# Kernel optimization log

Hardware: AMD Instinct MI355X
Metric: run time of the kernel (lower is better)

The kernel has to match this reference:

```python
import jax, jax.numpy as jnp
import numpy as np

N_NODES, N_EDGES, D_FEAT, HIDDEN, N_CLASSES = 100000, 3200000, 128, 16, 40


def setup_inputs() -> dict:
    key = jax.random.key(0)
    ks = jax.random.split(key, 6)
    x = jax.random.normal(ks[0], (N_NODES, D_FEAT), dtype=jnp.float32)
    edge_index = jax.random.randint(ks[1], (2, N_EDGES), 0, N_NODES, dtype=jnp.int32)
    # SAGEConv params: lin_l (aggregated neighbors, with bias), lin_r (root, no bias)
    W_l = jax.random.normal(ks[2], (D_FEAT, HIDDEN), dtype=jnp.float32) / np.sqrt(D_FEAT)
    b_l = jnp.zeros((HIDDEN,), jnp.float32)
    W_r = jax.random.normal(ks[3], (D_FEAT, HIDDEN), dtype=jnp.float32) / np.sqrt(D_FEAT)
    # final Linear(hidden, num_classes)
    W3 = jax.random.normal(ks[4], (HIDDEN, N_CLASSES), dtype=jnp.float32) / np.sqrt(HIDDEN)
    b3 = jnp.zeros((N_CLASSES,), jnp.float32)
    return {"x": x, "edge_index": edge_index, "W_l": W_l, "b_l": b_l,
            "W_r": W_r, "W3": W3, "b3": b3}


def reference(x, edge_index, W_l, b_l, W_r, W3, b3):
    N = x.shape[0]
    src, dst = edge_index[0], edge_index[1]
    # mean aggregation of source features onto target nodes (PyG source_to_target)
    agg = jax.ops.segment_sum(x[src], dst, num_segments=N)            # [N, F]
    deg = jax.ops.segment_sum(jnp.ones_like(dst, dtype=x.dtype), dst, num_segments=N)
    mean = agg / jnp.maximum(deg, 1.0)[:, None]                        # zero-in-degree -> 0
    # SAGEConv: lin_l(mean) + lin_r(x)
    h = mean @ W_l + b_l + x @ W_r                                     # [N, 16]
    h = jax.nn.relu(h)
    logits = h @ W3 + b3                                               # [N, C]
    return jax.nn.log_softmax(logits, axis=1)
```

## Files before the change

### kernel.cpp

```cpp
#include <hip/hip_runtime.h>
#include <hip/hip_bf16.h>

#define D_FEAT 128
#define HIDDEN 16
#define NCLS 40
#define EPB 4096
#define QSCALE 32.0f
#define QBIAS  8.0f

typedef unsigned int uint;

__device__ __forceinline__ void fma4(float4& a, float s, const float4 w) {
  a.x += s * w.x; a.y += s * w.y; a.z += s * w.z; a.w += s * w.w;
}

__global__ __launch_bounds__(256) void p1lin_kernel(
    const int* __restrict__ src, const int* __restrict__ dst,
    int* __restrict__ gcur1, int* __restrict__ buf1,
    int E, int C, int R1, int nb1,
    const float* __restrict__ x,
    const float* __restrict__ Wl, const float* __restrict__ Wr,
    uint* __restrict__ ylb, float* __restrict__ yr, int N) {
  __shared__ __align__(16) char smem[20880];
  int tid = threadIdx.x;

  if ((int)blockIdx.x < nb1) {
    int* lbuf  = (int*)smem;
    unsigned char* skey = (unsigned char*)(smem + 16384);
    int* lh    = (int*)(smem + 20480);
    int* loff  = lh + 32;
    int* gbase = loff + 33;
    if (tid < 32) lh[tid] = 0;
    __syncthreads();

    int base = blockIdx.x * EPB;
    int key[16], rnk[16], rec[16];
#pragma unroll
    for (int j = 0; j < 16; ++j) {
      int e = base + j * 256 + tid;
      bool ok = e < E;
      int d = ok ? dst[e] : 0;
      int s = ok ? src[e] : 0;
      key[j] = ok ? (d >> 12) : -1;
      rec[j] = s | ((d & 4095) << 17);
      if (ok) rnk[j] = atomicAdd(&lh[key[j]], 1);
    }
    __syncthreads();

    if (tid < 64) {
      int v = (tid < 32) ? lh[tid] : 0;
      int inc = v;
#pragma unroll
      for (int dd = 1; dd < 32; dd <<= 1) {
        int t = __shfl_up(inc, dd);
        if ((int)tid >= dd) inc += t;
      }
      if (tid < 32) {
        loff[tid] = inc - v;
        gbase[tid] = (v && tid < C) ? atomicAdd(&gcur1[tid], v) : 0;
      }
    }
    __syncthreads();

#pragma unroll
    for (int j = 0; j < 16; ++j) {
      if (key[j] >= 0) {
        int p = loff[key[j]] + rnk[j];
        lbuf[p] = rec[j];
        skey[p] = (unsigned char)key[j];
      }
    }
    __syncthreads();

    int tot = min(EPB, E - base);
    for (int i = tid; i < tot; i += 256) {
      int r = lbuf[i];
      int k = skey[i];
      int gp = gbase[k] + (i - loff[k]);
      if (gp < R1) buf1[(size_t)k * R1 + gp] = r;
    }
  } else {
    float* sW = (float*)smem;
    const float4* sWf4 = (const float4*)smem;

    for (int i = tid; i < 4096; i += 256) {
      int k = i >> 5, c = i & 31;
      sW[i] = (c < 16) ? Wl[k * 16 + c] : Wr[k * 16 + (c - 16)];
    }
    __syncthreads();

    int row0 = ((int)blockIdx.x - nb1) * 128;
    int quad = tid & 7, rg = tid >> 3;
    int r0 = row0 + rg * 4;
    int rr0 = min(r0 + 0, N - 1), rr1 = min(r0 + 1, N - 1);
    int rr2 = min(r0 + 2, N - 1), rr3 = min(r0 + 3, N - 1);
    const float* xp0 = x + (size_t)rr0 * D_FEAT;
    const float* xp1 = x + (size_t)rr1 * D_FEAT;
    const float* xp2 = x + (size_t)rr2 * D_FEAT;
    const float* xp3 = x + (size_t)rr3 * D_FEAT;

    float4 acc0 = {0,0,0,0}, acc1 = {0,0,0,0}, acc2 = {0,0,0,0}, acc3 = {0,0,0,0};
#pragma unroll 4
    for (int k4 = 0; k4 < 32; ++k4) {
      float4 x0 = *(const float4*)(xp0 + k4 * 4);
      float4 x1 = *(const float4*)(xp1 + k4 * 4);
      float4 x2 = *(const float4*)(xp2 + k4 * 4);
      float4 x3 = *(const float4*)(xp3 + k4 * 4);
      float4 w0 = sWf4[(k4 * 4 + 0) * 8 + quad];
      fma4(acc0, x0.x, w0); fma4(acc1, x1.x, w0);
      fma4(acc2, x2.x, w0); fma4(acc3, x3.x, w0);
      float4 w1 = sWf4[(k4 * 4 + 1) * 8 + quad];
      fma4(acc0, x0.y, w1); fma4(acc1, x1.y, w1);
      fma4(acc2, x2.y, w1); fma4(acc3, x3.y, w1);
      float4 w2 = sWf4[(k4 * 4 + 2) * 8 + quad];
      fma4(acc0, x0.z, w2); fma4(acc1, x1.z, w2);
      fma4(acc2, x2.z, w2); fma4(acc3, x3.z, w2);
      float4 w3 = sWf4[(k4 * 4 + 3) * 8 + quad];
      fma4(acc0, x0.w, w3); fma4(acc1, x1.w, w3);
      fma4(acc2, x2.w, w3); fma4(acc3, x3.w, w3);
    }

    float4 accs[4] = {acc0, acc1, acc2, acc3};
    if (quad < 4) {
#pragma unroll
      for (int r = 0; r < 4; ++r) {
        if (r0 + r < N) {
          float4 a = accs[r];
          int q0 = __float2int_rn((fminf(fmaxf(a.x, -7.9f), 7.9f) + QBIAS) * QSCALE);
          int q1 = __float2int_rn((fminf(fmaxf(a.y, -7.9f), 7.9f) + QBIAS) * QSCALE);
          int q2 = __float2int_rn((fminf(fmaxf(a.z, -7.9f), 7.9f) + QBIAS) * QSCALE);
          int q3 = __float2int_rn((fminf(fmaxf(a.w, -7.9f), 7.9f) + QBIAS) * QSCALE);
          uint2 pk;
          pk.x = (uint)q0 | ((uint)q1 << 16);
          pk.y = (uint)q2 | ((uint)q3 << 16);
          *(uint2*)(ylb + (size_t)(r0 + r) * 8 + quad * 2) = pk;
        }
      }
    } else {
#pragma unroll
      for (int r = 0; r < 4; ++r) {
        if (r0 + r < N)
          *(float4*)(yr + (size_t)(r0 + r) * 16 + (quad - 4) * 4) = accs[r];
      }
    }
  }
}

__global__ __launch_bounds__(256) void pass2_kernel(
    const int* __restrict__ buf1, const int* __restrict__ gcur1,
    int* __restrict__ gcur, int* __restrict__ packed,
    int C, int R1, int RF, int chunks) {
  __shared__ int lbuf[EPB];
  __shared__ int lh[32], loff[32], gbase[32];

  int c = blockIdx.x / chunks;
  int chunk = blockIdx.x - c * chunks;
  int cnt1 = min(gcur1[c], R1);
  int base = chunk * EPB;
  int tot = cnt1 - base;
  if (tot <= 0) return;
  tot = min(tot, EPB);

  int tid = threadIdx.x;
  if (tid < 32) lh[tid] = 0;
  __syncthreads();

  const int* in = buf1 + (size_t)c * R1 + base;
  int key[16], rnk[16], rec[16];
#pragma unroll
  for (int j = 0; j < 16; ++j) {
    int i = j * 256 + tid;
    bool ok = i < tot;
    int r = ok ? in[i] : 0;
    key[j] = ok ? ((r >> 24) & 31) : -1;
    rec[j] = r;
    if (ok) rnk[j] = atomicAdd(&lh[key[j]], 1);
  }
  __syncthreads();

  if (tid < 64) {
    int v = (tid < 32) ? lh[tid] : 0;
    int inc = v;
#pragma unroll
    for (int dd = 1; dd < 32; dd <<= 1) {
      int t = __shfl_up(inc, dd);
      if ((int)tid >= dd) inc += t;
    }
    if (tid < 32) {
      loff[tid] = inc - v;
      gbase[tid] = v ? atomicAdd(&gcur[c * 32 + tid], v) : 0;
    }
  }
  __syncthreads();

#pragma unroll
  for (int j = 0; j < 16; ++j)
    if (key[j] >= 0) lbuf[loff[key[j]] + rnk[j]] = rec[j];
  __syncthreads();

  for (int i = tid; i < tot; i += 256) {
    int r = lbuf[i];
    int k = (r >> 24) & 31;
    int gp = gbase[k] + (i - loff[k]);
    if (gp < RF) {
      int d12 = (r >> 17) & 4095;
      packed[(size_t)(c * 32 + k) * RF + gp] =
          (r & 0x1FFFF) | ((d12 & 127) << 20);
    }
  }
}

__global__ __launch_bounds__(1024) void baggrf_kernel(
    const uint* __restrict__ ylb, const int* __restrict__ packed,
    const int* __restrict__ gcur, const float* __restrict__ yr,
    const float* __restrict__ bl, const float* __restrict__ W3,
    const float* __restrict__ b3, float* __restrict__ out,
    int N, int RF) {
  __shared__ uint sagg[128 * 9];
  __shared__ int sdeg[128];
  __shared__ float syr[128 * 16];
  __shared__ float sW3[16 * NCLS];
  __shared__ float sb3[NCLS];
  __shared__ float sbl[16];
  int tid = threadIdx.x;
  int b = blockIdx.x;
  int node0 = b * 128;

  for (int i = tid; i < 128 * 9; i += 1024) sagg[i] = 0u;
  if (tid < 128) sdeg[tid] = 0;
  if (tid >= 384 && tid < 1024) sW3[tid - 384] = W3[tid - 384];
  if (tid < NCLS) sb3[tid] = b3[tid];
  if (tid >= 64 && tid < 80) sbl[tid - 64] = bl[tid - 64];
  __syncthreads();

  int cnt = min(gcur[b], RF);
  int lo = b * RF, hi = lo + cnt;
  for (int e0 = lo + tid; e0 < hi; e0 += 4096) {
    int e1 = e0 + 1024, e2 = e0 + 2048, e3 = e0 + 3072;
    bool h1 = e1 < hi, h2 = e2 < hi, h3 = e3 < hi;
    int p0 = packed[e0];
    int p1 = packed[h1 ? e1 : e0];
    int p2 = packed[h2 ? e2 : e0];
    int p3 = packed[h3 ? e3 : e0];
    int s0 = p0 & 0xFFFFF, d0 = (p0 >> 20) & 127;
    int s1 = p1 & 0xFFFFF, d1 = (p1 >> 20) & 127;
    int s2 = p2 & 0xFFFFF, d2 = (p2 >> 20) & 127;
    int s3 = p3 & 0xFFFFF, d3 = (p3 >> 20) & 127;
    const uint4* q0 = (const uint4*)(ylb + (size_t)s0 * 8);
    const uint4* q1 = (const uint4*)(ylb + (size_t)s1 * 8);
    const uint4* q2 = (const uint4*)(ylb + (size_t)s2 * 8);
    const uint4* q3 = (const uint4*)(ylb + (size_t)s3 * 8);
    uint4 a0 = q0[0], a1 = q0[1];
    uint4 b0 = q1[0], b1 = q1[1];
    uint4 c0 = q2[0], c1 = q2[1];
    uint4 e4 = q3[0], e5 = q3[1];

    uint* ip0 = &sagg[d0 * 9];
    atomicAdd(ip0 + 0, a0.x); atomicAdd(ip0 + 1, a0.y);
    atomicAdd(ip0 + 2, a0.z); atomicAdd(ip0 + 3, a0.w);
    atomicAdd(ip0 + 4, a1.x); atomicAdd(ip0 + 5, a1.y);
    atomicAdd(ip0 + 6, a1.z); atomicAdd(ip0 + 7, a1.w);
    atomicAdd(&sdeg[d0], 1);
    if (h1) {
      uint* ip = &sagg[d1 * 9];
      atomicAdd(ip + 0, b0.x); atomicAdd(ip + 1, b0.y);
      atomicAdd(ip + 2, b0.z); atomicAdd(ip + 3, b0.w);
      atomicAdd(ip + 4, b1.x); atomicAdd(ip + 5, b1.y);
      atomicAdd(ip + 6, b1.z); atomicAdd(ip + 7, b1.w);
      atomicAdd(&sdeg[d1], 1);
    }
    if (h2) {
      uint* ip = &sagg[d2 * 9];
      atomicAdd(ip + 0, c0.x); atomicAdd(ip + 1, c0.y);
      atomicAdd(ip + 2, c0.z); atomicAdd(ip + 3, c0.w);
      atomicAdd(ip + 4, c1.x); atomicAdd(ip + 5, c1.y);
      atomicAdd(ip + 6, c1.z); atomicAdd(ip + 7, c1.w);
      atomicAdd(&sdeg[d2], 1);
    }
    if (h3) {
      uint* ip = &sagg[d3 * 9];
      atomicAdd(ip + 0, e4.x); atomicAdd(ip + 1, e4.y);
      atomicAdd(ip + 2, e4.z); atomicAdd(ip + 3, e4.w);
      atomicAdd(ip + 4, e5.x); atomicAdd(ip + 5, e5.y);
      atomicAdd(ip + 6, e5.z); atomicAdd(ip + 7, e5.w);
      atomicAdd(&sdeg[d3], 1);
    }
  }

  int nvalid = min(128, N - node0);
  if (nvalid > 0) {
    int tot16 = nvalid * 16;
    for (int i = tid; i < tot16; i += 1024)
      syr[i] = yr[(size_t)node0 * 16 + i];
  }
  __syncthreads();

  int node = tid >> 3, q = tid & 7;
  int n = node0 + node;
  if (n < N) {
    int dg = sdeg[node];
    float bsub = (QBIAS * QSCALE) * (float)dg;
    float inv = 1.0f / (QSCALE * fmaxf((float)dg, 1.0f));
    float h[16];
#pragma unroll
    for (int j = 0; j < 8; ++j) {
      uint s = sagg[node * 9 + j];
      float v0 = ((float)(s & 0xFFFFu) - bsub) * inv;
      float v1 = ((float)(s >> 16) - bsub) * inv;
      h[2 * j]     = fmaxf(v0 + sbl[2 * j]     + syr[node * 16 + 2 * j], 0.f);
      h[2 * j + 1] = fmaxf(v1 + sbl[2 * j + 1] + syr[node * 16 + 2 * j + 1], 0.f);
    }
    float lg[5];
#pragma unroll
    for (int j = 0; j < 5; ++j) lg[j] = sb3[q * 5 + j];
#pragma unroll
    for (int k = 0; k < 16; ++k) {
      float hv = h[k];
#pragma unroll
      for (int j = 0; j < 5; ++j) lg[j] += hv * sW3[k * NCLS + q * 5 + j];
    }
    float m = lg[0];
#pragma unroll
    for (int j = 1; j < 5; ++j) m = fmaxf(m, lg[j]);
#pragma unroll
    for (int dd = 1; dd < 8; dd <<= 1) m = fmaxf(m, __shfl_xor(m, dd));
    float s = 0.f;
#pragma unroll
    for (int j = 0; j < 5; ++j) s += __expf(lg[j] - m);
#pragma unroll
    for (int dd = 1; dd < 8; dd <<= 1) s += __shfl_xor(s, dd);
    float lse = m + __logf(s);
    float* op = out + (size_t)n * NCLS + q * 5;
#pragma unroll
    for (int j = 0; j < 5; ++j) op[j] = lg[j] - lse;
  }
}

extern "C" void kernel_launch(void* const* d_in, const int* in_sizes, int n_in,
                              void* d_out, int out_size, void* d_ws, size_t ws_size,
                              hipStream_t stream) {
  const float* x   = (const float*)d_in[0];
  const int* eidx  = (const int*)d_in[1];
  const float* Wl  = (const float*)d_in[2];
  const float* bl  = (const float*)d_in[3];
  const float* Wr  = (const float*)d_in[4];
  const float* W3  = (const float*)d_in[5];
  const float* b3  = (const float*)d_in[6];
  float* out = (float*)d_out;

  int N = in_sizes[0] / D_FEAT;
  int E = in_sizes[1] / 2;
  const int* src = eidx;
  const int* dst = eidx + E;

  int C = (N + 4095) >> 12;
  int chunks = (E / C) / EPB + 2;
  int R1 = chunks * EPB;
  int Bf = C * 32;
  int B = (N + 127) >> 7;
  long long m = (long long)E * 128 / N;
  int RF = (int)((m + m / 8 + 511) / 512 * 512);

  size_t n16 = (size_t)N * 16;
  uint* ylb   = (uint*)d_ws;
  float* yr   = (float*)(ylb + (size_t)N * 8);
  int* gcur   = (int*)(yr + n16);
  int* gcur1  = gcur + Bf;
  int* buf1   = gcur1 + C;
  int* packed = buf1 + (size_t)C * R1;

  hipMemsetAsync(gcur, 0, (size_t)(Bf + C) * sizeof(int), stream);

  int nb1 = (E + EPB - 1) / EPB;
  int nblin = (N + 127) / 128;
  p1lin_kernel<<<nb1 + nblin, 256, 0, stream>>>(src, dst, gcur1, buf1,
                                                E, C, R1, nb1,
                                                x, Wl, Wr, ylb, yr, N);

  pass2_kernel<<<C * chunks, 256, 0, stream>>>(buf1, gcur1, gcur, packed,
                                               C, R1, RF, chunks);

  baggrf_kernel<<<B, 1024, 0, stream>>>(ylb, packed, gcur, yr, bl, W3, b3,
                                        out, N, RF);
}
```

Measured before the change: 98.86 us.

## Split fused partition/linear kernel into separate pass1 and lin kernels

Undoes the fusion of the edge-partition pass and the dense linear projection, launching them as two separate kernels. The partition kernel now precomputes each edge's global destination index in shared memory instead of storing a byte key and recomputing offsets in the scatter loop. The lin kernel gets a launch-bounds occupancy hint. Separate launches drop the shared-memory union and let each kernel use its own resources, at the cost of losing concurrency between the two phases and adding one launch.

```diff
diff --git a/kernel.cpp b/kernel.cpp
--- a/kernel.cpp
+++ b/kernel.cpp
@@ -14,134 +14,130 @@
   a.x += s * w.x; a.y += s * w.y; a.z += s * w.z; a.w += s * w.w;
 }
 
-__global__ __launch_bounds__(256) void p1lin_kernel(
+__global__ __launch_bounds__(256) void pass1_kernel(
     const int* __restrict__ src, const int* __restrict__ dst,
     int* __restrict__ gcur1, int* __restrict__ buf1,
-    int E, int C, int R1, int nb1,
+    int E, int C, int R1) {
+  __shared__ int lh[32], loff[32], gbase[32];
+  __shared__ int lbuf[EPB];
+  __shared__ int ldst[EPB];
+  int tid = threadIdx.x;
+  if (tid < 32) lh[tid] = 0;
+  __syncthreads();
+
+  int base = blockIdx.x * EPB;
+  int key[16], rnk[16], rec[16];
+#pragma unroll
+  for (int j = 0; j < 16; ++j) {
+    int e = base + j * 256 + tid;
+    bool ok = e < E;
+    int d = ok ? dst[e] : 0;
+    int s = ok ? src[e] : 0;
+    key[j] = ok ? (d >> 12) : -1;
+    rec[j] = s | ((d & 4095) << 17);
+    if (ok) rnk[j] = atomicAdd(&lh[key[j]], 1);
+  }
+  __syncthreads();
+
+  if (tid < 64) {
+    int v = (tid < 32) ? lh[tid] : 0;
+    int inc = v;
+#pragma unroll
+    for (int dd = 1; dd < 32; dd <<= 1) {
+      int t = __shfl_up(inc, dd);
+      if ((int)tid >= dd) inc += t;
+    }
+    if (tid < 32) {
+      loff[tid] = inc - v;
+      gbase[tid] = (v && tid < C) ? atomicAdd(&gcur1[tid], v) : 0;
+    }
+  }
+  __syncthreads();
+
+#pragma unroll
+  for (int j = 0; j < 16; ++j) {
+    if (key[j] >= 0) {
+      int p = loff[key[j]] + rnk[j];
+      lbuf[p] = rec[j];
+      int gp = gbase[key[j]] + rnk[j];
+      ldst[p] = (gp < R1) ? key[j] * R1 + gp : -1;
+    }
+  }
+  __syncthreads();
+
+  int tot = min(EPB, E - base);
+  for (int i = tid; i < tot; i += 256) {
+    int di = ldst[i];
+    if (di >= 0) buf1[di] = lbuf[i];
+  }
+}
+
+__global__ __launch_bounds__(256, 6) void lin_kernel(
     const float* __restrict__ x,
     const float* __restrict__ Wl, const float* __restrict__ Wr,
     uint* __restrict__ ylb, float* __restrict__ yr, int N) {
-  __shared__ __align__(16) char smem[20880];
+  __shared__ float sW[4096];
+  const float4* sWf4 = (const float4*)sW;
   int tid = threadIdx.x;
 
-  if ((int)blockIdx.x < nb1) {
-    int* lbuf  = (int*)smem;
-    unsigned char* skey = (unsigned char*)(smem + 16384);
-    int* lh    = (int*)(smem + 20480);
-    int* loff  = lh + 32;
-    int* gbase = loff + 33;
-    if (tid < 32) lh[tid] = 0;
-    __syncthreads();
-
-    int base = blockIdx.x * EPB;
-    int key[16], rnk[16], rec[16];
-#pragma unroll
-    for (int j = 0; j < 16; ++j) {
-      int e = base + j * 256 + tid;
-      bool ok = e < E;
-      int d = ok ? dst[e] : 0;
-      int s = ok ? src[e] : 0;
-      key[j] = ok ? (d >> 12) : -1;
-      rec[j] = s | ((d & 4095) << 17);
-      if (ok) rnk[j] = atomicAdd(&lh[key[j]], 1);
-    }
-    __syncthreads();
-
-    if (tid < 64) {
-      int v = (tid < 32) ? lh[tid] : 0;
-      int inc = v;
-#pragma unroll
-      for (int dd = 1; dd < 32; dd <<= 1) {
-        int t = __shfl_up(inc, dd);
-        if ((int)tid >= dd) inc += t;
+  for (int i = tid; i < 4096; i += 256) {
+    int k = i >> 5, c = i & 31;
+    sW[i] = (c < 16) ? Wl[k * 16 + c] : Wr[k * 16 + (c - 16)];
+  }
+  __syncthreads();
+
+  int row0 = blockIdx.x * 128;
+  int quad = tid & 7, rg = tid >> 3;
+  int r0 = row0 + rg * 4;
+  int rr0 = min(r0 + 0, N - 1), rr1 = min(r0 + 1, N - 1);
+  int rr2 = min(r0 + 2, N - 1), rr3 = min(r0 + 3, N - 1);
+  const float* xp0 = x + (size_t)rr0 * D_FEAT;
+  const float* xp1 = x + (size_t)rr1 * D_FEAT;
+  const float* xp2 = x + (size_t)rr2 * D_FEAT;
+  const float* xp3 = x + (size_t)rr3 * D_FEAT;
+
+  float4 acc0 = {0,0,0,0}, acc1 = {0,0,0,0}, acc2 = {0,0,0,0}, acc3 = {0,0,0,0};
+#pragma unroll 4
+  for (int k4 = 0; k4 < 32; ++k4) {
+    float4 x0 = *(const float4*)(xp0 + k4 * 4);
+    float4 x1 = *(const float4*)(xp1 + k4 * 4);
+    float4 x2 = *(const float4*)(xp2 + k4 * 4);
+    float4 x3 = *(const float4*)(xp3 + k4 * 4);
+    float4 w0 = sWf4[(k4 * 4 + 0) * 8 + quad];
+    fma4(acc0, x0.x, w0); fma4(acc1, x1.x, w0);
+    fma4(acc2, x2.x, w0); fma4(acc3, x3.x, w0);
+    float4 w1 = sWf4[(k4 * 4 + 1) * 8 + quad];
+    fma4(acc0, x0.y, w1); fma4(acc1, x1.y, w1);
+    fma4(acc2, x2.y, w1); fma4(acc3, x3.y, w1);
+    float4 w2 = sWf4[(k4 * 4 + 2) * 8 + quad];
+    fma4(acc0, x0.z, w2); fma4(acc1, x1.z, w2);
+    fma4(acc2, x2.z, w2); fma4(acc3, x3.z, w2);
+    float4 w3 = sWf4[(k4 * 4 + 3) * 8 + quad];
+    fma4(acc0, x0.w, w3); fma4(acc1, x1.w, w3);
+    fma4(acc2, x2.w, w3); fma4(acc3, x3.w, w3);
+  }
+
+  float4 accs[4] = {acc0, acc1, acc2, acc3};
+  if (quad < 4) {
+#pragma unroll
+    for (int r = 0; r < 4; ++r) {
+      if (r0 + r < N) {
+        float4 a = accs[r];
+        int q0 = __float2int_rn((fminf(fmaxf(a.x, -7.9f), 7.9f) + QBIAS) * QSCALE);
+        int q1 = __float2int_rn((fminf(fmaxf(a.y, -7.9f), 7.9f) + QBIAS) * QSCALE);
+        int q2 = __float2int_rn((fminf(fmaxf(a.z, -7.9f), 7.9f) + QBIAS) * QSCALE);
+        int q3 = __float2int_rn((fminf(fmaxf(a.w, -7.9f), 7.9f) + QBIAS) * QSCALE);
+        uint2 pk;
+        pk.x = (uint)q0 | ((uint)q1 << 16);
+        pk.y = (uint)q2 | ((uint)q3 << 16);
+        *(uint2*)(ylb + (size_t)(r0 + r) * 8 + quad * 2) = pk;
       }
-      if (tid < 32) {
-        loff[tid] = inc - v;
-        gbase[tid] = (v && tid < C) ? atomicAdd(&gcur1[tid], v) : 0;
-      }
-    }
-    __syncthreads();
-
-#pragma unroll
-    for (int j = 0; j < 16; ++j) {
-      if (key[j] >= 0) {
-        int p = loff[key[j]] + rnk[j];
-        lbuf[p] = rec[j];
-        skey[p] = (unsigned char)key[j];
-      }
-    }
-    __syncthreads();
-
-    int tot = min(EPB, E - base);
-    for (int i = tid; i < tot; i += 256) {
-      int r = lbuf[i];
-      int k = skey[i];
-      int gp = gbase[k] + (i - loff[k]);
-      if (gp < R1) buf1[(size_t)k * R1 + gp] = r;
     }
   } else {
-    float* sW = (float*)smem;
-    const float4* sWf4 = (const float4*)smem;
-
-    for (int i = tid; i < 4096; i += 256) {
-      int k = i >> 5, c = i & 31;
-      sW[i] = (c < 16) ? Wl[k * 16 + c] : Wr[k * 16 + (c - 16)];
-    }
-    __syncthreads();
-
-    int row0 = ((int)blockIdx.x - nb1) * 128;
-    int quad = tid & 7, rg = tid >> 3;
-    int r0 = row0 + rg * 4;
-    int rr0 = min(r0 + 0, N - 1), rr1 = min(r0 + 1, N - 1);
-    int rr2 = min(r0 + 2, N - 1), rr3 = min(r0 + 3, N - 1);
-    const float* xp0 = x + (size_t)rr0 * D_FEAT;
-    const float* xp1 = x + (size_t)rr1 * D_FEAT;
-    const float* xp2 = x + (size_t)rr2 * D_FEAT;
-    const float* xp3 = x + (size_t)rr3 * D_FEAT;
-
-    float4 acc0 = {0,0,0,0}, acc1 = {0,0,0,0}, acc2 = {0,0,0,0}, acc3 = {0,0,0,0};
-#pragma unroll 4
-    for (int k4 = 0; k4 < 32; ++k4) {
-      float4 x0 = *(const float4*)(xp0 + k4 * 4);
-      float4 x1 = *(const float4*)(xp1 + k4 * 4);
-      float4 x2 = *(const float4*)(xp2 + k4 * 4);
-      float4 x3 = *(const float4*)(xp3 + k4 * 4);
-      float4 w0 = sWf4[(k4 * 4 + 0) * 8 + quad];
-      fma4(acc0, x0.x, w0); fma4(acc1, x1.x, w0);
-      fma4(acc2, x2.x, w0); fma4(acc3, x3.x, w0);
-      float4 w1 = sWf4[(k4 * 4 + 1) * 8 + quad];
-      fma4(acc0, x0.y, w1); fma4(acc1, x1.y, w1);
-      fma4(acc2, x2.y, w1); fma4(acc3, x3.y, w1);
-      float4 w2 = sWf4[(k4 * 4 + 2) * 8 + quad];
-      fma4(acc0, x0.z, w2); fma4(acc1, x1.z, w2);
-      fma4(acc2, x2.z, w2); fma4(acc3, x3.z, w2);
-      float4 w3 = sWf4[(k4 * 4 + 3) * 8 + quad];
-      fma4(acc0, x0.w, w3); fma4(acc1, x1.w, w3);
-      fma4(acc2, x2.w, w3); fma4(acc3, x3.w, w3);
-    }
-
-    float4 accs[4] = {acc0, acc1, acc2, acc3};
-    if (quad < 4) {
-#pragma unroll
-      for (int r = 0; r < 4; ++r) {
-        if (r0 + r < N) {
-          float4 a = accs[r];
-          int q0 = __float2int_rn((fminf(fmaxf(a.x, -7.9f), 7.9f) + QBIAS) * QSCALE);
-          int q1 = __float2int_rn((fminf(fmaxf(a.y, -7.9f), 7.9f) + QBIAS) * QSCALE);
-          int q2 = __float2int_rn((fminf(fmaxf(a.z, -7.9f), 7.9f) + QBIAS) * QSCALE);
-          int q3 = __float2int_rn((fminf(fmaxf(a.w, -7.9f), 7.9f) + QBIAS) * QSCALE);
-          uint2 pk;
-          pk.x = (uint)q0 | ((uint)q1 << 16);
-          pk.y = (uint)q2 | ((uint)q3 << 16);
-          *(uint2*)(ylb + (size_t)(r0 + r) * 8 + quad * 2) = pk;
-        }
-      }
-    } else {
-#pragma unroll
-      for (int r = 0; r < 4; ++r) {
-        if (r0 + r < N)
-          *(float4*)(yr + (size_t)(r0 + r) * 16 + (quad - 4) * 4) = accs[r];
-      }
+#pragma unroll
+    for (int r = 0; r < 4; ++r) {
+      if (r0 + r < N)
+        *(float4*)(yr + (size_t)(r0 + r) * 16 + (quad - 4) * 4) = accs[r];
     }
   }
 }
@@ -372,10 +368,10 @@
   hipMemsetAsync(gcur, 0, (size_t)(Bf + C) * sizeof(int), stream);
 
   int nb1 = (E + EPB - 1) / EPB;
+  pass1_kernel<<<nb1, 256, 0, stream>>>(src, dst, gcur1, buf1, E, C, R1);
+
   int nblin = (N + 127) / 128;
-  p1lin_kernel<<<nb1 + nblin, 256, 0, stream>>>(src, dst, gcur1, buf1,
-                                                E, C, R1, nb1,
-                                                x, Wl, Wr, ylb, yr, N);
+  lin_kernel<<<nblin, 256, 0, stream>>>(x, Wl, Wr, ylb, yr, N);
 
   pass2_kernel<<<C * chunks, 256, 0, stream>>>(buf1, gcur1, gcur, packed,
                                                C, R1, RF, chunks);
```

Result: slower. 105.4 us (+6.6%).

## Fuse three-kernel pipeline into one persistent cooperative kernel with grid syncs

Applied to the files above, without the earlier changes.

Replaces the memset and the three separate launches (bucket pass 1 plus linear, pass 2, aggregate-and-finalize) with a single cooperative persistent kernel. It uses 1024-thread blocks that loop over work items and separates the stages with grid-wide syncs. Tile sizes change as well: EPB doubles and linear tiles grow to 512 rows. This removes launch gaps and the memset, but adds grid.sync overhead, caps the grid at 512 blocks, and 1024-thread blocks may reduce occupancy or load balance.

```diff
diff --git a/kernel.cpp b/kernel.cpp
--- a/kernel.cpp
+++ b/kernel.cpp
@@ -1,10 +1,12 @@
 #include <hip/hip_runtime.h>
+#include <hip/hip_cooperative_groups.h>
 #include <hip/hip_bf16.h>
 
+namespace cg = cooperative_groups;
+
 #define D_FEAT 128
-#define HIDDEN 16
 #define NCLS 40
-#define EPB 4096
+#define EPB 8192
 #define QSCALE 32.0f
 #define QBIAS  8.0f
 
@@ -14,35 +16,182 @@
   a.x += s * w.x; a.y += s * w.y; a.z += s * w.z; a.w += s * w.w;
 }
 
-__global__ __launch_bounds__(256) void p1lin_kernel(
+__global__ __launch_bounds__(1024, 8) void mega_kernel(
     const int* __restrict__ src, const int* __restrict__ dst,
-    int* __restrict__ gcur1, int* __restrict__ buf1,
-    int E, int C, int R1, int nb1,
     const float* __restrict__ x,
     const float* __restrict__ Wl, const float* __restrict__ Wr,
-    uint* __restrict__ ylb, float* __restrict__ yr, int N) {
-  __shared__ __align__(16) char smem[20880];
+    const float* __restrict__ bl, const float* __restrict__ W3,
+    const float* __restrict__ b3,
+    uint* __restrict__ ylb, float* __restrict__ yr,
+    int* __restrict__ gcur, int* __restrict__ gcur1,
+    int* __restrict__ buf1, int* __restrict__ packed,
+    float* __restrict__ out,
+    int N, int E, int C, int R1, int RF, int chunks2,
+    int nb1, int nblin, int nItem2, int nItem3) {
+  cg::grid_group grid = cg::this_grid();
+  __shared__ __align__(16) char smem[41472];
   int tid = threadIdx.x;
-
-  if ((int)blockIdx.x < nb1) {
-    int* lbuf  = (int*)smem;
-    unsigned char* skey = (unsigned char*)(smem + 16384);
-    int* lh    = (int*)(smem + 20480);
-    int* loff  = lh + 32;
-    int* gbase = loff + 33;
+  int bid = blockIdx.x;
+  int nBlk = gridDim.x;
+
+  if (bid == 0) {
+    int tot = C * 32 + C;
+    for (int i = tid; i < tot; i += 1024) gcur[i] = 0;
+  }
+  grid.sync();
+
+  int nItem1 = nb1 + nblin;
+  for (int it = bid; it < nItem1; it += nBlk) {
+    if (it < nb1) {
+      int* lbuf = (int*)smem;
+      unsigned char* skey = (unsigned char*)(smem + 32768);
+      int* lh = (int*)(smem + 40960);
+      int* loff = lh + 32;
+      int* gbase = loff + 32;
+      if (tid < 32) lh[tid] = 0;
+      __syncthreads();
+
+      int base = it * EPB;
+      int key[8], rnk[8], rec[8];
+#pragma unroll
+      for (int j = 0; j < 8; ++j) {
+        int e = base + j * 1024 + tid;
+        bool ok = e < E;
+        int d = ok ? dst[e] : 0;
+        int s = ok ? src[e] : 0;
+        key[j] = ok ? (d >> 12) : -1;
+        rec[j] = s | ((d & 4095) << 17);
+        if (ok) rnk[j] = atomicAdd(&lh[key[j]], 1);
+      }
+      __syncthreads();
+
+      if (tid < 64) {
+        int v = (tid < 32) ? lh[tid] : 0;
+        int inc = v;
+#pragma unroll
+        for (int dd = 1; dd < 32; dd <<= 1) {
+          int t = __shfl_up(inc, dd);
+          if ((int)tid >= dd) inc += t;
+        }
+        if (tid < 32) {
+          loff[tid] = inc - v;
+          gbase[tid] = (v && tid < C) ? atomicAdd(&gcur1[tid], v) : 0;
+        }
+      }
+      __syncthreads();
+
+#pragma unroll
+      for (int j = 0; j < 8; ++j) {
+        if (key[j] >= 0) {
+          int p = loff[key[j]] + rnk[j];
+          lbuf[p] = rec[j];
+          skey[p] = (unsigned char)key[j];
+        }
+      }
+      __syncthreads();
+
+      int tot = min(EPB, E - base);
+      for (int i = tid; i < tot; i += 1024) {
+        int r = lbuf[i];
+        int k = skey[i];
+        int gp = gbase[k] + (i - loff[k]);
+        if (gp < R1) buf1[(size_t)k * R1 + gp] = r;
+      }
+      __syncthreads();
+    } else {
+      float* sW = (float*)smem;
+      const float4* sWf4 = (const float4*)smem;
+      for (int i = tid; i < 4096; i += 1024) {
+        int k = i >> 5, c = i & 31;
+        sW[i] = (c < 16) ? Wl[k * 16 + c] : Wr[k * 16 + (c - 16)];
+      }
+      __syncthreads();
+
+      int row0 = (it - nb1) * 512;
+      int quad = tid & 7, rg = tid >> 3;
+      int r0 = row0 + rg * 4;
+      int rr0 = min(r0 + 0, N - 1), rr1 = min(r0 + 1, N - 1);
+      int rr2 = min(r0 + 2, N - 1), rr3 = min(r0 + 3, N - 1);
+      const float* xp0 = x + (size_t)rr0 * D_FEAT;
+      const float* xp1 = x + (size_t)rr1 * D_FEAT;
+      const float* xp2 = x + (size_t)rr2 * D_FEAT;
+      const float* xp3 = x + (size_t)rr3 * D_FEAT;
+
+      float4 acc0 = {0,0,0,0}, acc1 = {0,0,0,0};
+      float4 acc2 = {0,0,0,0}, acc3 = {0,0,0,0};
+#pragma unroll 4
+      for (int k4 = 0; k4 < 32; ++k4) {
+        float4 x0 = *(const float4*)(xp0 + k4 * 4);
+        float4 x1 = *(const float4*)(xp1 + k4 * 4);
+        float4 x2 = *(const float4*)(xp2 + k4 * 4);
+        float4 x3 = *(const float4*)(xp3 + k4 * 4);
+        float4 w0 = sWf4[(k4 * 4 + 0) * 8 + quad];
+        fma4(acc0, x0.x, w0); fma4(acc1, x1.x, w0);
+        fma4(acc2, x2.x, w0); fma4(acc3, x3.x, w0);
+        float4 w1 = sWf4[(k4 * 4 + 1) * 8 + quad];
+        fma4(acc0, x0.y, w1); fma4(acc1, x1.y, w1);
+        fma4(acc2, x2.y, w1); fma4(acc3, x3.y, w1);
+        float4 w2 = sWf4[(k4 * 4 + 2) * 8 + quad];
+        fma4(acc0, x0.z, w2); fma4(acc1, x1.z, w2);
+        fma4(acc2, x2.z, w2); fma4(acc3, x3.z, w2);
+        float4 w3 = sWf4[(k4 * 4 + 3) * 8 + quad];
+        fma4(acc0, x0.w, w3); fma4(acc1, x1.w, w3);
+        fma4(acc2, x2.w, w3); fma4(acc3, x3.w, w3);
+      }
+
+      float4 accs[4] = {acc0, acc1, acc2, acc3};
+      if (quad < 4) {
+#pragma unroll
+        for (int r = 0; r < 4; ++r) {
+          if (r0 + r < N) {
+            float4 a = accs[r];
+            int q0 = __float2int_rn((fminf(fmaxf(a.x, -7.9f), 7.9f) + QBIAS) * QSCALE);
+            int q1 = __float2int_rn((fminf(fmaxf(a.y, -7.9f), 7.9f) + QBIAS) * QSCALE);
+            int q2 = __float2int_rn((fminf(fmaxf(a.z, -7.9f), 7.9f) + QBIAS) * QSCALE);
+            int q3 = __float2int_rn((fminf(fmaxf(a.w, -7.9f), 7.9f) + QBIAS) * QSCALE);
+            uint2 pk;
+            pk.x = (uint)q0 | ((uint)q1 << 16);
+            pk.y = (uint)q2 | ((uint)q3 << 16);
+            *(uint2*)(ylb + (size_t)(r0 + r) * 8 + quad * 2) = pk;
+          }
+        }
+      } else {
+#pragma unroll
+        for (int r = 0; r < 4; ++r) {
+          if (r0 + r < N)
+            *(float4*)(yr + (size_t)(r0 + r) * 16 + (quad - 4) * 4) = accs[r];
+        }
+      }
+      __syncthreads();
+    }
+  }
+  grid.sync();
+
+  for (int it = bid; it < nItem2; it += nBlk) {
+    int c = it / chunks2;
+    int chunk = it - c * chunks2;
+    int cnt1 = min(gcur1[c], R1);
+    int base = chunk * EPB;
+    int tot = cnt1 - base;
+    if (tot <= 0) continue;
+    tot = min(tot, EPB);
+
+    int* lbuf = (int*)smem;
+    int* lh = (int*)(smem + 40960);
+    int* loff = lh + 32;
+    int* gbase = loff + 32;
     if (tid < 32) lh[tid] = 0;
     __syncthreads();
 
-    int base = blockIdx.x * EPB;
-    int key[16], rnk[16], rec[16];
-#pragma unroll
-    for (int j = 0; j < 16; ++j) {
-      int e = base + j * 256 + tid;
-      bool ok = e < E;
-      int d = ok ? dst[e] : 0;
-      int s = ok ? src[e] : 0;
-      key[j] = ok ? (d >> 12) : -1;
-      rec[j] = s | ((d & 4095) << 17);
+    const int* in = buf1 + (size_t)c * R1 + base;
+    int key[8], rnk[8], rec[8];
+#pragma unroll
+    for (int j = 0; j < 8; ++j) {
+      int i = j * 1024 + tid;
+      bool ok = i < tot;
+      int r = ok ? in[i] : 0;
+      key[j] = ok ? ((r >> 24) & 31) : -1;
+      rec[j] = r;
       if (ok) rnk[j] = atomicAdd(&lh[key[j]], 1);
     }
     __syncthreads();
@@ -57,290 +206,156 @@
       }
       if (tid < 32) {
         loff[tid] = inc - v;
-        gbase[tid] = (v && tid < C) ? atomicAdd(&gcur1[tid], v) : 0;
-      }
-    }
-    __syncthreads();
-
-#pragma unroll
-    for (int j = 0; j < 16; ++j) {
-      if (key[j] >= 0) {
-        int p = loff[key[j]] + rnk[j];
-        lbuf[p] = rec[j];
-        skey[p] = (unsigned char)key[j];
-      }
-    }
-    __syncthreads();
-
-    int tot = min(EPB, E - base);
-    for (int i = tid; i < tot; i += 256) {
+        gbase[tid] = v ? atomicAdd(&gcur[c * 32 + tid], v) : 0;
+      }
+    }
+    __syncthreads();
+
+#pragma unroll
+    for (int j = 0; j < 8; ++j)
+      if (key[j] >= 0) lbuf[loff[key[j]] + rnk[j]] = rec[j];
+    __syncthreads();
+
+    for (int i = tid; i < tot; i += 1024) {
       int r = lbuf[i];
-      int k = skey[i];
+      int k = (r >> 24) & 31;
       int gp = gbase[k] + (i - loff[k]);
-      if (gp < R1) buf1[(size_t)k * R1 + gp] = r;
-    }
-  } else {
-    float* sW = (float*)smem;
-    const float4* sWf4 = (const float4*)smem;
-
-    for (int i = tid; i < 4096; i += 256) {
-      int k = i >> 5, c = i & 31;
-      sW[i] = (c < 16) ? Wl[k * 16 + c] : Wr[k * 16 + (c - 16)];
-    }
-    __syncthreads();
-
-    int row0 = ((int)blockIdx.x - nb1) * 128;
-    int quad = tid & 7, rg = tid >> 3;
-    int r0 = row0 + rg * 4;
-    int rr0 = min(r0 + 0, N - 1), rr1 = min(r0 + 1, N - 1);
-    int rr2 = min(r0 + 2, N - 1), rr3 = min(r0 + 3, N - 1);
-    const float* xp0 = x + (size_t)rr0 * D_FEAT;
-    const float* xp1 = x + (size_t)rr1 * D_FEAT;
-    const float* xp2 = x + (size_t)rr2 * D_FEAT;
-    const float* xp3 = x + (size_t)rr3 * D_FEAT;
-
-    float4 acc0 = {0,0,0,0}, acc1 = {0,0,0,0}, acc2 = {0,0,0,0}, acc3 = {0,0,0,0};
-#pragma unroll 4
-    for (int k4 = 0; k4 < 32; ++k4) {
-      float4 x0 = *(const float4*)(xp0 + k4 * 4);
-      float4 x1 = *(const float4*)(xp1 + k4 * 4);
-      float4 x2 = *(const float4*)(xp2 + k4 * 4);
-      float4 x3 = *(const float4*)(xp3 + k4 * 4);
-      float4 w0 = sWf4[(k4 * 4 + 0) * 8 + quad];
-      fma4(acc0, x0.x, w0); fma4(acc1, x1.x, w0);
-      fma4(acc2, x2.x, w0); fma4(acc3, x3.x, w0);
-      float4 w1 = sWf4[(k4 * 4 + 1) * 8 + quad];
-      fma4(acc0, x0.y, w1); fma4(acc1, x1.y, w1);
-      fma4(acc2, x2.y, w1); fma4(acc3, x3.y, w1);
-      float4 w2 = sWf4[(k4 * 4 + 2) * 8 + quad];
-      fma4(acc0, x0.z, w2); fma4(acc1, x1.z, w2);
-      fma4(acc2, x2.z, w2); fma4(acc3, x3.z, w2);
-      float4 w3 = sWf4[(k4 * 4 + 3) * 8 + quad];
-      fma4(acc0, x0.w, w3); fma4(acc1, x1.w, w3);
-      fma4(acc2, x2.w, w3); fma4(acc3, x3.w, w3);
-    }
-
-    float4 accs[4] = {acc0, acc1, acc2, acc3};
-    if (quad < 4) {
-#pragma unroll
-      for (int r = 0; r < 4; ++r) {
-        if (r0 + r < N) {
-          float4 a = accs[r];
-          int q0 = __float2int_rn((fminf(fmaxf(a.x, -7.9f), 7.9f) + QBIAS) * QSCALE);
-          int q1 = __float2int_rn((fminf(fmaxf(a.y, -7.9f), 7.9f) + QBIAS) * QSCALE);
-          int q2 = __float2int_rn((fminf(fmaxf(a.z, -7.9f), 7.9f) + QBIAS) * QSCALE);
-          int q3 = __float2int_rn((fminf(fmaxf(a.w, -7.9f), 7.9f) + QBIAS) * QSCALE);
-          uint2 pk;
-          pk.x = (uint)q0 | ((uint)q1 << 16);
-          pk.y = (uint)q2 | ((uint)q3 << 16);
-          *(uint2*)(ylb + (size_t)(r0 + r) * 8 + quad * 2) = pk;
-        }
-      }
-    } else {
-#pragma unroll
-      for (int r = 0; r < 4; ++r) {
-        if (r0 + r < N)
-          *(float4*)(yr + (size_t)(r0 + r) * 16 + (quad - 4) * 4) = accs[r];
-      }
-    }
+      if (gp < RF) {
+        int d12 = (r >> 17) & 4095;
+        packed[(size_t)(c * 32 + k) * RF + gp] =
+            (r & 0x1FFFF) | ((d12 & 127) << 20);
+      }
+    }
+    __syncthreads();
   }
-}
-
-__global__ __launch_bounds__(256) void pass2_kernel(
-    const int* __restrict__ buf1, const int* __restrict__ gcur1,
-    int* __restrict__ gcur, int* __restrict__ packed,
-    int C, int R1, int RF, int chunks) {
-  __shared__ int lbuf[EPB];
-  __shared__ int lh[32], loff[32], gbase[32];
-
-  int c = blockIdx.x / chunks;
-  int chunk = blockIdx.x - c * chunks;
-  int cnt1 = min(gcur1[c], R1);
-  int base = chunk * EPB;
-  int tot = cnt1 - base;
-  if (tot <= 0) return;
-  tot = min(tot, EPB);
-
-  int tid = threadIdx.x;
-  if (tid < 32) lh[tid] = 0;
-  __syncthreads();
-
-  const int* in = buf1 + (size_t)c * R1 + base;
-  int key[16], rnk[16], rec[16];
-#pragma unroll
-  for (int j = 0; j < 16; ++j) {
-    int i = j * 256 + tid;
-    bool ok = i < tot;
-    int r = ok ? in[i] : 0;
-    key[j] = ok ? ((r >> 24) & 31) : -1;
-    rec[j] = r;
-    if (ok) rnk[j] = atomicAdd(&lh[key[j]], 1);
-  }
-  __syncthreads();
-
-  if (tid < 64) {
-    int v = (tid < 32) ? lh[tid] : 0;
-    int inc = v;
-#pragma unroll
-    for (int dd = 1; dd < 32; dd <<= 1) {
-      int t = __shfl_up(inc, dd);
-      if ((int)tid >= dd) inc += t;
-    }
-    if (tid < 32) {
-      loff[tid] = inc - v;
-      gbase[tid] = v ? atomicAdd(&gcur[c * 32 + tid], v) : 0;
-    }
-  }
-  __syncthreads();
-
-#pragma unroll
-  for (int j = 0; j < 16; ++j)
-    if (key[j] >= 0) lbuf[loff[key[j]] + rnk[j]] = rec[j];
-  __syncthreads();
-
-  for (int i = tid; i < tot; i += 256) {
-    int r = lbuf[i];
-    int k = (r >> 24) & 31;
-    int gp = gbase[k] + (i - loff[k]);
-    if (gp < RF) {
-      int d12 = (r >> 17) & 4095;
-      packed[(size_t)(c * 32 + k) * RF + gp] =
-          (r & 0x1FFFF) | ((d12 & 127) << 20);
-    }
-  }
-}
-
-__global__ __launch_bounds__(1024) void baggrf_kernel(
-    const uint* __restrict__ ylb, const int* __restrict__ packed,
-    const int* __restrict__ gcur, const float* __restrict__ yr,
-    const float* __restrict__ bl, const float* __restrict__ W3,
-    const float* __restrict__ b3, float* __restrict__ out,
-    int N, int RF) {
-  __shared__ uint sagg[128 * 9];
-  __shared__ int sdeg[128];
-  __shared__ float syr[128 * 16];
-  __shared__ float sW3[16 * NCLS];
-  __shared__ float sb3[NCLS];
-  __shared__ float sbl[16];
-  int tid = threadIdx.x;
-  int b = blockIdx.x;
-  int node0 = b * 128;
-
-  for (int i = tid; i < 128 * 9; i += 1024) sagg[i] = 0u;
-  if (tid < 128) sdeg[tid] = 0;
-  if (tid >= 384 && tid < 1024) sW3[tid - 384] = W3[tid - 384];
-  if (tid < NCLS) sb3[tid] = b3[tid];
-  if (tid >= 64 && tid < 80) sbl[tid - 64] = bl[tid - 64];
-  __syncthreads();
-
-  int cnt = min(gcur[b], RF);
-  int lo = b * RF, hi = lo + cnt;
-  for (int e0 = lo + tid; e0 < hi; e0 += 4096) {
-    int e1 = e0 + 1024, e2 = e0 + 2048, e3 = e0 + 3072;
-    bool h1 = e1 < hi, h2 = e2 < hi, h3 = e3 < hi;
-    int p0 = packed[e0];
-    int p1 = packed[h1 ? e1 : e0];
-    int p2 = packed[h2 ? e2 : e0];
-    int p3 = packed[h3 ? e3 : e0];
-    int s0 = p0 & 0xFFFFF, d0 = (p0 >> 20) & 127;
-    int s1 = p1 & 0xFFFFF, d1 = (p1 >> 20) & 127;
-    int s2 = p2 & 0xFFFFF, d2 = (p2 >> 20) & 127;
-    int s3 = p3 & 0xFFFFF, d3 = (p3 >> 20) & 127;
-    const uint4* q0 = (const uint4*)(ylb + (size_t)s0 * 8);
-    const uint4* q1 = (const uint4*)(ylb + (size_t)s1 * 8);
-    const uint4* q2 = (const uint4*)(ylb + (size_t)s2 * 8);
-    const uint4* q3 = (const uint4*)(ylb + (size_t)s3 * 8);
-    uint4 a0 = q0[0], a1 = q0[1];
-    uint4 b0 = q1[0], b1 = q1[1];
-    uint4 c0 = q2[0], c1 = q2[1];
-    uint4 e4 = q3[0], e5 = q3[1];
-
-    uint* ip0 = &sagg[d0 * 9];
-    atomicAdd(ip0 + 0, a0.x); atomicAdd(ip0 + 1, a0.y);
-    atomicAdd(ip0 + 2, a0.z); atomicAdd(ip0 + 3, a0.w);
-    atomicAdd(ip0 + 4, a1.x); atomicAdd(ip0 + 5, a1.y);
-    atomicAdd(ip0 + 6, a1.z); atomicAdd(ip0 + 7, a1.w);
-    atomicAdd(&sdeg[d0], 1);
-    if (h1) {
-      uint* ip = &sagg[d1 * 9];
-      atomicAdd(ip + 0, b0.x); atomicAdd(ip + 1, b0.y);
-      atomicAdd(ip + 2, b0.z); atomicAdd(ip + 3, b0.w);
-      atomicAdd(ip + 4, b1.x); atomicAdd(ip + 5, b1.y);
-      atomicAdd(ip + 6, b1.z); atomicAdd(ip + 7, b1.w);
-      atomicAdd(&sdeg[d1], 1);
-    }
-    if (h2) {
-      uint* ip = &sagg[d2 * 9];
-      atomicAdd(ip + 0, c0.x); atomicAdd(ip + 1, c0.y);
-      atomicAdd(ip + 2, c0.z); atomicAdd(ip + 3, c0.w);
-      atomicAdd(ip + 4, c1.x); atomicAdd(ip + 5, c1.y);
-      atomicAdd(ip + 6, c1.z); atomicAdd(ip + 7, c1.w);
-      atomicAdd(&sdeg[d2], 1);
-    }
-    if (h3) {
-      uint* ip = &sagg[d3 * 9];
-      atomicAdd(ip + 0, e4.x); atomicAdd(ip + 1, e4.y);
-      atomicAdd(ip + 2, e4.z); atomicAdd(ip + 3, e4.w);
-      atomicAdd(ip + 4, e5.x); atomicAdd(ip + 5, e5.y);
-      atomicAdd(ip + 6, e5.z); atomicAdd(ip + 7, e5.w);
-      atomicAdd(&sdeg[d3], 1);
-    }
-  }
-
-  int nvalid = min(128, N - node0);
-  if (nvalid > 0) {
-    int tot16 = nvalid * 16;
-    for (int i = tid; i < tot16; i += 1024)
-      syr[i] = yr[(size_t)node0 * 16 + i];
-  }
-  __syncthreads();
-
-  int node = tid >> 3, q = tid & 7;
-  int n = node0 + node;
-  if (n < N) {
-    int dg = sdeg[node];
-    float bsub = (QBIAS * QSCALE) * (float)dg;
-    float inv = 1.0f / (QSCALE * fmaxf((float)dg, 1.0f));
-    float h[16];
-#pragma unroll
-    for (int j = 0; j < 8; ++j) {
-      uint s = sagg[node * 9 + j];
-      float v0 = ((float)(s & 0xFFFFu) - bsub) * inv;
-      float v1 = ((float)(s >> 16) - bsub) * inv;
-      h[2 * j]     = fmaxf(v0 + sbl[2 * j]     + syr[node * 16 + 2 * j], 0.f);
-      h[2 * j + 1] = fmaxf(v1 + sbl[2 * j + 1] + syr[node * 16 + 2 * j + 1], 0.f);
-    }
-    float lg[5];
-#pragma unroll
-    for (int j = 0; j < 5; ++j) lg[j] = sb3[q * 5 + j];
-#pragma unroll
-    for (int k = 0; k < 16; ++k) {
-      float hv = h[k];
-#pragma unroll
-      for (int j = 0; j < 5; ++j) lg[j] += hv * sW3[k * NCLS + q * 5 + j];
-    }
-    float m = lg[0];
-#pragma unroll
-    for (int j = 1; j < 5; ++j) m = fmaxf(m, lg[j]);
-#pragma unroll
-    for (int dd = 1; dd < 8; dd <<= 1) m = fmaxf(m, __shfl_xor(m, dd));
-    float s = 0.f;
-#pragma unroll
-    for (int j = 0; j < 5; ++j) s += __expf(lg[j] - m);
-#pragma unroll
-    for (int dd = 1; dd < 8; dd <<= 1) s += __shfl_xor(s, dd);
-    float lse = m + __logf(s);
-    float* op = out + (size_t)n * NCLS + q * 5;
-#pragma unroll
-    for (int j = 0; j < 5; ++j) op[j] = lg[j] - lse;
+  grid.sync();
+
+  for (int it = bid; it < nItem3; it += nBlk) {
+    uint* sagg = (uint*)smem;
+    int* sdeg = (int*)(smem + 4608);
+    float* syr = (float*)(smem + 5120);
+    float* sW3 = (float*)(smem + 13312);
+    float* sb3 = (float*)(smem + 15872);
+    float* sbl = (float*)(smem + 16032);
+    int node0 = it * 128;
+
+    for (int i = tid; i < 128 * 9; i += 1024) sagg[i] = 0u;
+    if (tid < 128) sdeg[tid] = 0;
+    if (tid >= 384 && tid < 1024) sW3[tid - 384] = W3[tid - 384];
+    if (tid < NCLS) sb3[tid] = b3[tid];
+    if (tid >= 64 && tid < 80) sbl[tid - 64] = bl[tid - 64];
+    __syncthreads();
+
+    int cnt = min(gcur[it], RF);
+    int lo = it * RF, hi = lo + cnt;
+    for (int e0 = lo + tid; e0 < hi; e0 += 4096) {
+      int e1 = e0 + 1024, e2 = e0 + 2048, e3 = e0 + 3072;
+      bool h1 = e1 < hi, h2 = e2 < hi, h3 = e3 < hi;
+      int p0 = packed[e0];
+      int p1 = packed[h1 ? e1 : e0];
+      int p2 = packed[h2 ? e2 : e0];
+      int p3 = packed[h3 ? e3 : e0];
+      int s0 = p0 & 0xFFFFF, d0 = (p0 >> 20) & 127;
+      int s1 = p1 & 0xFFFFF, d1 = (p1 >> 20) & 127;
+      int s2 = p2 & 0xFFFFF, d2 = (p2 >> 20) & 127;
+      int s3 = p3 & 0xFFFFF, d3 = (p3 >> 20) & 127;
+      const uint4* q0 = (const uint4*)(ylb + (size_t)s0 * 8);
+      const uint4* q1 = (const uint4*)(ylb + (size_t)s1 * 8);
+      const uint4* q2 = (const uint4*)(ylb + (size_t)s2 * 8);
+      const uint4* q3 = (const uint4*)(ylb + (size_t)s3 * 8);
+      uint4 a0 = q0[0], a1 = q0[1];
+      uint4 b0 = q1[0], b1 = q1[1];
+      uint4 c0 = q2[0], c1 = q2[1];
+      uint4 e4 = q3[0], e5 = q3[1];
+
+      uint* ip0 = &sagg[d0 * 9];
+      atomicAdd(ip0 + 0, a0.x); atomicAdd(ip0 + 1, a0.y);
+      atomicAdd(ip0 + 2, a0.z); atomicAdd(ip0 + 3, a0.w);
+      atomicAdd(ip0 + 4, a1.x); atomicAdd(ip0 + 5, a1.y);
+      atomicAdd(ip0 + 6, a1.z); atomicAdd(ip0 + 7, a1.w);
+      atomicAdd(&sdeg[d0], 1);
+      if (h1) {
+        uint* ip = &sagg[d1 * 9];
+        atomicAdd(ip + 0, b0.x); atomicAdd(ip + 1, b0.y);
+        atomicAdd(ip + 2, b0.z); atomicAdd(ip + 3, b0.w);
+        atomicAdd(ip + 4, b1.x); atomicAdd(ip + 5, b1.y);
+        atomicAdd(ip + 6, b1.z); atomicAdd(ip + 7, b1.w);
+        atomicAdd(&sdeg[d1], 1);
+      }
+      if (h2) {
+        uint* ip = &sagg[d2 * 9];
+        atomicAdd(ip + 0, c0.x); atomicAdd(ip + 1, c0.y);
+        atomicAdd(ip + 2, c0.z); atomicAdd(ip + 3, c0.w);
+        atomicAdd(ip + 4, c1.x); atomicAdd(ip + 5, c1.y);
+        atomicAdd(ip + 6, c1.z); atomicAdd(ip + 7, c1.w);
+        atomicAdd(&sdeg[d2], 1);
+      }
+      if (h3) {
+        uint* ip = &sagg[d3 * 9];
+        atomicAdd(ip + 0, e4.x); atomicAdd(ip + 1, e4.y);
+        atomicAdd(ip + 2, e4.z); atomicAdd(ip + 3, e4.w);
+        atomicAdd(ip + 4, e5.x); atomicAdd(ip + 5, e5.y);
+        atomicAdd(ip + 6, e5.z); atomicAdd(ip + 7, e5.w);
+        atomicAdd(&sdeg[d3], 1);
+      }
+    }
+
+    int nvalid = min(128, N - node0);
+    if (nvalid > 0) {
+      int tot16 = nvalid * 16;
+      for (int i = tid; i < tot16; i += 1024)
+        syr[i] = yr[(size_t)node0 * 16 + i];
+    }
+    __syncthreads();
+
+    int node = tid >> 3, q = tid & 7;
+    int n = node0 + node;
+    if (n < N) {
+      int dg = sdeg[node];
+      float bsub = (QBIAS * QSCALE) * (float)dg;
+      float inv = 1.0f / (QSCALE * fmaxf((float)dg, 1.0f));
+      float h[16];
+#pragma unroll
+      for (int j = 0; j < 8; ++j) {
+        uint s = sagg[node * 9 + j];
+        float v0 = ((float)(s & 0xFFFFu) - bsub) * inv;
+        float v1 = ((float)(s >> 16) - bsub) * inv;
+        h[2 * j]     = fmaxf(v0 + sbl[2 * j]     + syr[node * 16 + 2 * j], 0.f);
+        h[2 * j + 1] = fmaxf(v1 + sbl[2 * j + 1] + syr[node * 16 + 2 * j + 1], 0.f);
+      }
+      float lg[5];
+#pragma unroll
+      for (int j = 0; j < 5; ++j) lg[j] = sb3[q * 5 + j];
+#pragma unroll
+      for (int k = 0; k < 16; ++k) {
+        float hv = h[k];
+#pragma unroll
+        for (int j = 0; j < 5; ++j) lg[j] += hv * sW3[k * NCLS + q * 5 + j];
+      }
+      float m = lg[0];
+#pragma unroll
+      for (int j = 1; j < 5; ++j) m = fmaxf(m, lg[j]);
+#pragma unroll
+      for (int dd = 1; dd < 8; dd <<= 1) m = fmaxf(m, __shfl_xor(m, dd));
+      float s = 0.f;
+#pragma unroll
+      for (int j = 0; j < 5; ++j) s += __expf(lg[j] - m);
+#pragma unroll
+      for (int dd = 1; dd < 8; dd <<= 1) s += __shfl_xor(s, dd);
+      float lse = m + __logf(s);
+      float* op = out + (size_t)n * NCLS + q * 5;
+#pragma unroll
+      for (int j = 0; j < 5; ++j) op[j] = lg[j] - lse;
+    }
+    __syncthreads();
   }
 }
 
 extern "C" void kernel_launch(void* const* d_in, const int* in_sizes, int n_in,
                               void* d_out, int out_size, void* d_ws, size_t ws_size,
                               hipStream_t stream) {
+  const int* eidx  = (const int*)d_in[1];
   const float* x   = (const float*)d_in[0];
-  const int* eidx  = (const int*)d_in[1];
   const float* Wl  = (const float*)d_in[2];
   const float* bl  = (const float*)d_in[3];
   const float* Wr  = (const float*)d_in[4];
@@ -354,12 +369,18 @@
   const int* dst = eidx + E;
 
   int C = (N + 4095) >> 12;
-  int chunks = (E / C) / EPB + 2;
-  int R1 = chunks * EPB;
+  long long full = (long long)E * 4096 / N;
+  int chunks2 = (int)((full + EPB + EPB - 1) / EPB);
+  int R1 = chunks2 * EPB;
   int Bf = C * 32;
   int B = (N + 127) >> 7;
   long long m = (long long)E * 128 / N;
   int RF = (int)((m + m / 8 + 511) / 512 * 512);
+
+  int nb1 = (E + EPB - 1) / EPB;
+  int nblin = (N + 511) / 512;
+  int nItem2 = C * chunks2;
+  int nItem3 = B;
 
   size_t n16 = (size_t)N * 16;
   uint* ylb   = (uint*)d_ws;
@@ -369,17 +390,20 @@
   int* buf1   = gcur1 + C;
   int* packed = buf1 + (size_t)C * R1;
 
-  hipMemsetAsync(gcur, 0, (size_t)(Bf + C) * sizeof(int), stream);
-
-  int nb1 = (E + EPB - 1) / EPB;
-  int nblin = (N + 127) / 128;
-  p1lin_kernel<<<nb1 + nblin, 256, 0, stream>>>(src, dst, gcur1, buf1,
-                                                E, C, R1, nb1,
-                                                x, Wl, Wr, ylb, yr, N);
-
-  pass2_kernel<<<C * chunks, 256, 0, stream>>>(buf1, gcur1, gcur, packed,
-                                               C, R1, RF, chunks);
-
-  baggrf_kernel<<<B, 1024, 0, stream>>>(ylb, packed, gcur, yr, bl, W3, b3,
-                                        out, N, RF);
+  int mbpc = 0;
+  hipOccupancyMaxActiveBlocksPerMultiprocessor(&mbpc, mega_kernel, 1024, 0);
+  if (mbpc < 1) mbpc = 1;
+  int grid = mbpc * 256;
+  if (grid > 512) grid = 512;
+
+  void* kargs[] = {
+    (void*)&src, (void*)&dst, (void*)&x, (void*)&Wl, (void*)&Wr,
+    (void*)&bl, (void*)&W3, (void*)&b3,
+    (void*)&ylb, (void*)&yr, (void*)&gcur, (void*)&gcur1,
+    (void*)&buf1, (void*)&packed, (void*)&out,
+    (void*)&N, (void*)&E, (void*)&C, (void*)&R1, (void*)&RF, (void*)&chunks2,
+    (void*)&nb1, (void*)&nblin, (void*)&nItem2, (void*)&nItem3 };
+
+  hipLaunchCooperativeKernel(mega_kernel, dim3(grid), dim3(1024),
+                             kargs, 0u, stream);
 }
```

New measurement: 209.7 us. +112.1%, slower.
